# Optimization experiments

Measured on AMD Instinct MI355X. Metric: run time of the kernel, lower is better.

Reference implementation:

```python
import jax, jax.numpy as jnp
import numpy as np

L, H, E, CUTOFF = 3, 128, 20, 5.0
N_NODES, N_EDGES = 10000, 160000
NUM_EMBED = 119


def _linear(key, fin, fout):
    kw, kb = jax.random.split(key)
    s = 1.0 / np.sqrt(fin)
    W = jax.random.uniform(kw, (fin, fout), minval=-s, maxval=s, dtype=jnp.float32)
    b = jax.random.uniform(kb, (fout,), minval=-s, maxval=s, dtype=jnp.float32)
    return W, b


def _stack(key, fin, fout):
    Ws, bs = zip(*[_linear(k, fin, fout) for k in jax.random.split(key, L)])
    return jnp.stack(Ws), jnp.stack(bs)


def setup_inputs() -> dict:
    key = jax.random.key(0)
    ks = jax.random.split(key, 14)
    z = jax.random.randint(ks[0], (N_NODES,), 0, NUM_EMBED)
    edge = jax.random.randint(ks[1], (N_EDGES, 2), 0, N_NODES)
    edge_diff = jax.random.normal(ks[2], (N_EDGES, 3), dtype=jnp.float32) * 1.5
    edge_dist = jnp.linalg.norm(edge_diff, axis=-1) + 1e-2  # consistent unit vectors, strictly > 0
    embed = jax.random.normal(ks[3], (NUM_EMBED, H), dtype=jnp.float32)
    msg_filter_w, msg_filter_b = _stack(ks[4], E, 3 * H)
    msg_w1, msg_b1 = _stack(ks[5], H, H)
    msg_w2, msg_b2 = _stack(ks[6], H, 3 * H)
    upd_U_w, upd_U_b = _stack(ks[7], H, H)
    upd_V_w, upd_V_b = _stack(ks[8], H, H)
    upd_w1, upd_b1 = _stack(ks[9], 2 * H, H)
    upd_w2, upd_b2 = _stack(ks[10], H, 3 * H)
    ro_w1, ro_b1 = _linear(ks[11], H, H)
    ro_w2, ro_b2 = _linear(ks[12], H, H)
    return dict(z=z, edge=edge, edge_diff=edge_diff, edge_dist=edge_dist, embed=embed,
                msg_filter_w=msg_filter_w, msg_filter_b=msg_filter_b,
                msg_w1=msg_w1, msg_b1=msg_b1, msg_w2=msg_w2, msg_b2=msg_b2,
                upd_U_w=upd_U_w, upd_U_b=upd_U_b, upd_V_w=upd_V_w, upd_V_b=upd_V_b,
                upd_w1=upd_w1, upd_b1=upd_b1, upd_w2=upd_w2, upd_b2=upd_b2,
                ro_w1=ro_w1, ro_b1=ro_b1, ro_w2=ro_w2, ro_b2=ro_b2)


def _silu(x):
    return x * jax.nn.sigmoid(x)


def reference(z, edge, edge_diff, edge_dist, embed,
              msg_filter_w, msg_filter_b, msg_w1, msg_b1, msg_w2, msg_b2,
              upd_U_w, upd_U_b, upd_V_w, upd_V_b, upd_w1, upd_b1, upd_w2, upd_b2,
              ro_w1, ro_b1, ro_w2, ro_b2):
    N = z.shape[0]
    pi = jnp.asarray(np.pi, dtype=edge_dist.dtype)
    # sinc radial basis: sin(n*pi*d/cutoff)/d, n=1..E  -> [E_edges, E]
    n = jnp.arange(1, E + 1, dtype=edge_dist.dtype)
    rbf = jnp.sin(edge_dist[:, None] * n * pi / CUTOFF) / edge_dist[:, None]
    # cosine cutoff [E_edges]
    fcut = jnp.where(edge_dist < CUTOFF, 0.5 * (jnp.cos(pi * edge_dist / CUTOFF) + 1.0), 0.0)
    unit = edge_diff / edge_dist[:, None]  # [E_edges, 3]
    src = edge[:, 1]
    dst = edge[:, 0]

    node_scalar = embed[z]                                       # [N, H]
    node_vector = jnp.zeros((N, 3, H), dtype=edge_diff.dtype)    # [N, 3, H]

    for l in range(L):
        # --- message ---
        filter_w = (rbf @ msg_filter_w[l] + msg_filter_b[l]) * fcut[:, None]   # [E_edges, 3H]
        scalar_out = _silu(node_scalar @ msg_w1[l] + msg_b1[l]) @ msg_w2[l] + msg_b2[l]  # [N, 3H]
        filter_out = filter_w * scalar_out[src]                                 # gather + mul
        gate_sv, gate_ev, msg_s = jnp.split(filter_out, 3, axis=1)
        msg_v = node_vector[src] * gate_sv[:, None, :] + gate_ev[:, None, :] * unit[:, :, None]
        node_scalar = node_scalar + jax.ops.segment_sum(msg_s, dst, num_segments=N)
        node_vector = node_vector + jax.ops.segment_sum(msg_v, dst, num_segments=N)
        # --- update ---
        Uv = node_vector @ upd_U_w[l] + upd_U_b[l]   # [N, 3, H]
        Vv = node_vector @ upd_V_w[l] + upd_V_b[l]
        Vv_norm = jnp.linalg.norm(Vv, axis=1)        # [N, H]
        mlp_in = jnp.concatenate((Vv_norm, node_scalar), axis=1)
        mlp_out = _silu(mlp_in @ upd_w1[l] + upd_b1[l]) @ upd_w2[l] + upd_b2[l]
        a_vv, a_sv, a_ss = jnp.split(mlp_out, 3, axis=1)
        node_vector = node_vector + a_vv[:, None, :] * Uv
        node_scalar = node_scalar + a_sv * jnp.sum(Uv * Vv, axis=1) + a_ss

    # readout MLP
    return _silu(node_scalar @ ro_w1 + ro_b1) @ ro_w2 + ro_b2
```

## Files before the change

### kernel.cpp

```cpp
#include <hip/hip_runtime.h>
#include <hip/hip_bf16.h>

typedef __hip_bfloat16 bf16;
typedef __attribute__((ext_vector_type(8))) short bf16x8;
typedef __attribute__((ext_vector_type(4))) float f32x4;

#define H 128
#define F3H 384
#define E_RBF 20
#define NLAYER 3

__device__ __forceinline__ float silu_f(float x) { return x / (1.0f + __expf(-x)); }
__device__ __forceinline__ float b2f(bf16 x) { return __bfloat162float(x); }

constexpr float PI_F = 3.14159265358979323846f;
constexpr float CUT = 5.0f;

__global__ __launch_bounds__(256) void csr_hist(
    const int* __restrict__ edge, int* __restrict__ cnt, int nE) {
  int e = blockIdx.x * blockDim.x + threadIdx.x;
  if (e < nE) atomicAdd(&cnt[edge[2 * e]], 1);
}

__global__ __launch_bounds__(256) void csr_scan(
    const int* __restrict__ cnt, int* __restrict__ rowstart, int* __restrict__ cur, int N) {
  __shared__ int part[256];
  int t = threadIdx.x;
  int chunk = (N + 255) / 256;
  int lo = t * chunk; if (lo > N) lo = N;
  int hi = lo + chunk; if (hi > N) hi = N;
  int s = 0;
  for (int i = lo; i < hi; i++) s += cnt[i];
  part[t] = s;
  __syncthreads();
  if (t == 0) {
    int r = 0;
    for (int i = 0; i < 256; i++) { int v = part[i]; part[i] = r; r += v; }
  }
  __syncthreads();
  int r = part[t];
  for (int i = lo; i < hi; i++) { rowstart[i] = r; cur[i] = r; r += cnt[i]; }
}

__global__ __launch_bounds__(256) void csr_fill(
    const int* __restrict__ edge, int* __restrict__ cur, int* __restrict__ elist, int nE) {
  int e = blockIdx.x * blockDim.x + threadIdx.x;
  if (e < nE) {
    int d = edge[2 * e];
    int p = atomicAdd(&cur[d], 1);
    elist[p] = e;
  }
}

__global__ __launch_bounds__(256) void edge_pack(
    const int* __restrict__ elist, const int* __restrict__ edge,
    const float* __restrict__ edist, const float* __restrict__ ediff,
    int* __restrict__ srcs, float* __restrict__ geo, int nE) {
  int j = blockIdx.x * blockDim.x + threadIdx.x;
  if (j >= nE) return;
  int e = elist[j];
  srcs[j] = edge[2 * e + 1];
  float d = edist[e];
  float inv = 1.0f / d;
  float th = d * (PI_F / CUT);
  float s1 = sinf(th), c1 = cosf(th);
  float fc = (d < CUT) ? 0.5f * (c1 + 1.0f) : 0.0f;
  float* g = geo + (size_t)j * 24;
  float twoc = 2.0f * c1;
  float skp = 0.0f, sk = s1;
  #pragma unroll
  for (int k = 0; k < E_RBF; k++) {
    g[k] = sk * inv * fc;
    float nx = twoc * sk - skp;
    skp = sk; sk = nx;
  }
  g[20] = ediff[3 * (size_t)e] * inv;
  g[21] = ediff[3 * (size_t)e + 1] * inv;
  g[22] = ediff[3 * (size_t)e + 2] * inv;
  g[23] = fc;
}

__global__ __launch_bounds__(H) void node_init(
    const int* __restrict__ z, const float* __restrict__ embed,
    float* __restrict__ ns, bf16* __restrict__ ns16, int N) {
  int i = blockIdx.x;
  int h = threadIdx.x;
  float v = embed[(size_t)z[i] * H + h];
  ns[(size_t)i * H + h] = v;
  ns16[(size_t)i * H + h] = __float2bfloat16(v);
}

__global__ __launch_bounds__(256) void pack_w(
    const float* __restrict__ Wu, const float* __restrict__ Wv,
    bf16* __restrict__ wp) {
  int t = blockIdx.x * blockDim.x + threadIdx.x;
  if (t >= 3 * 2 * 4 * 8 * 64) return;
  int lane = t & 63;
  int c    = (t >> 6) & 7;
  int kb   = (t >> 9) & 3;
  int mat  = (t >> 11) & 1;
  int l    = t >> 12;
  const float* src = (mat ? Wv : Wu) + (size_t)l * H * H;
  bf16* dst = wp + ((size_t)(l * 2 + mat) * 16384) + (((kb * 8 + c) * 64 + lane) * 8);
  int quad = lane >> 4;
  int n = c * 16 + (lane & 15);
  #pragma unroll
  for (int j = 0; j < 8; j++) {
    int k = kb * 32 + quad * 8 + j;
    dst[j] = __float2bfloat16(src[(size_t)k * H + n]);
  }
}

__global__ __launch_bounds__(256) void pack_b(
    const float* __restrict__ src, bf16* __restrict__ dst,
    int K, int ncols, int L) {
  int kblocks = K >> 5, ncols16 = ncols >> 4;
  int total = L * kblocks * ncols16 * 64;
  int t = blockIdx.x * blockDim.x + threadIdx.x;
  if (t >= total) return;
  int lane = t & 63;
  int idx = t >> 6;
  int c = idx % ncols16; idx /= ncols16;
  int kb = idx % kblocks; idx /= kblocks;
  int l = idx;
  const float* s = src + (size_t)l * K * ncols;
  bf16* d = dst + (size_t)l * K * ncols + (((kb * ncols16 + c) * 64 + lane) * 8);
  int quad = lane >> 4;
  int n = c * 16 + (lane & 15);
  #pragma unroll
  for (int j = 0; j < 8; j++) {
    int k = kb * 32 + quad * 8 + j;
    d[j] = __float2bfloat16(s[(size_t)k * ncols + n]);
  }
}

__global__ __launch_bounds__(256) void mlp_msg(
    const bf16* __restrict__ A, const bf16* __restrict__ Wp1,
    const float* __restrict__ b1, const bf16* __restrict__ Wp2,
    const float* __restrict__ b2, bf16* __restrict__ so, int M) {
  __shared__ bf16 m1l[32][136];
  int wave = threadIdx.x >> 6, lane = threadIdx.x & 63;
  int rowg = wave >> 1, ch = wave & 1;
  int r0 = blockIdx.x * 32 + rowg * 16;
  int quad = lane >> 4, nn = lane & 15;
  int arow = r0 + nn; if (arow >= M) arow = M - 1;
  f32x4 acc[4] = {};
  for (int kb = 0; kb < 4; kb++) {
    bf16x8 af = *(const bf16x8*)&A[(size_t)arow * H + kb * 32 + quad * 8];
    #pragma unroll
    for (int c = 0; c < 4; c++) {
      int cg = ch * 4 + c;
      bf16x8 bw = *(const bf16x8*)&Wp1[(((kb * 8 + cg) * 64) + lane) * 8];
      acc[c] = __builtin_amdgcn_mfma_f32_16x16x32_bf16(af, bw, acc[c], 0, 0, 0);
    }
  }
  #pragma unroll
  for (int c = 0; c < 4; c++) {
    int n = (ch * 4 + c) * 16 + nn;
    float bb = b1[n];
    #pragma unroll
    for (int r = 0; r < 4; r++) {
      int lr = rowg * 16 + quad * 4 + r;
      m1l[lr][n] = __float2bfloat16(silu_f(acc[c][r] + bb));
    }
  }
  __syncthreads();
  f32x4 a0[4] = {}, a1[4] = {}, a2[4] = {};
  for (int kb = 0; kb < 4; kb++) {
    bf16x8 af = *(const bf16x8*)&m1l[rowg * 16 + nn][kb * 32 + quad * 8];
    #pragma unroll
    for (int c = 0; c < 4; c++) {
      int cg = ch * 4 + c;
      bf16x8 b0 = *(const bf16x8*)&Wp2[(((kb * 24 + cg) * 64) + lane) * 8];
      bf16x8 b1v = *(const bf16x8*)&Wp2[(((kb * 24 + cg + 8) * 64) + lane) * 8];
      bf16x8 b2v = *(const bf16x8*)&Wp2[(((kb * 24 + cg + 16) * 64) + lane) * 8];
      a0[c] = __builtin_amdgcn_mfma_f32_16x16x32_bf16(af, b0, a0[c], 0, 0, 0);
      a1[c] = __builtin_amdgcn_mfma_f32_16x16x32_bf16(af, b1v, a1[c], 0, 0, 0);
      a2[c] = __builtin_amdgcn_mfma_f32_16x16x32_bf16(af, b2v, a2[c], 0, 0, 0);
    }
  }
  #pragma unroll
  for (int c = 0; c < 4; c++) {
    int n = (ch * 4 + c) * 16 + nn;
    float bb0 = b2[n], bb1 = b2[H + n], bb2 = b2[2 * H + n];
    #pragma unroll
    for (int r = 0; r < 4; r++) {
      int row = r0 + quad * 4 + r;
      if (row < M) {
        so[(size_t)row * F3H + n]           = __float2bfloat16(a0[c][r] + bb0);
        so[(size_t)row * F3H + H + n]       = __float2bfloat16(a1[c][r] + bb1);
        so[(size_t)row * F3H + 2 * H + n]   = __float2bfloat16(a2[c][r] + bb2);
      }
    }
  }
}

__global__ __launch_bounds__(384) void uv_upd(
    const bf16* __restrict__ A, const bf16* __restrict__ Wpuv,
    const float* __restrict__ bu, const float* __restrict__ bv,
    const bf16* __restrict__ nsmsg,
    const bf16* __restrict__ Wp1, const float* __restrict__ b1,
    const bf16* __restrict__ Wp2, const float* __restrict__ b2,
    float* __restrict__ ns, bf16* __restrict__ ns16,
    float* __restrict__ nv, bf16* __restrict__ nvb16, int N) {
  __shared__ float Uv_l[96][132];
  __shared__ float Vv_l[96][132];
  __shared__ bf16 vn_l[32][136];
  __shared__ bf16 m1l[32][136];
  int wave = threadIdx.x >> 6;
  int lane = threadIdx.x & 63;
  int quad = lane >> 4, nn = lane & 15;
  int M3 = 3 * N;

  {
    int r0 = blockIdx.x * 96 + wave * 16;
    int arow = r0 + nn; if (arow >= M3) arow = M3 - 1;
    f32x4 accu[8] = {};
    f32x4 accv[8] = {};
    for (int kb = 0; kb < 4; kb++) {
      bf16x8 af = *(const bf16x8*)&A[(size_t)arow * H + kb * 32 + quad * 8];
      #pragma unroll
      for (int c = 0; c < 8; c++) {
        bf16x8 bfu = *(const bf16x8*)&Wpuv[(((kb * 8 + c) * 64) + lane) * 8];
        bf16x8 bfv = *(const bf16x8*)&Wpuv[16384 + (((kb * 8 + c) * 64) + lane) * 8];
        accu[c] = __builtin_amdgcn_mfma_f32_16x16x32_bf16(af, bfu, accu[c], 0, 0, 0);
        accv[c] = __builtin_amdgcn_mfma_f32_16x16x32_bf16(af, bfv, accv[c], 0, 0, 0);
      }
    }
    #pragma unroll
    for (int c = 0; c < 8; c++) {
      int n = c * 16 + nn;
      float bub = bu[n], bvb = bv[n];
      #pragma unroll
      for (int r = 0; r < 4; r++) {
        int lr = wave * 16 + quad * 4 + r;
        Uv_l[lr][n] = accu[c][r] + bub;
        Vv_l[lr][n] = accv[c][r] + bvb;
      }
    }
  }
  __syncthreads();

  for (int t = threadIdx.x; t < 32 * H; t += 384) {
    int node = t >> 7, hh = t & 127;
    float v0 = Vv_l[node * 3][hh];
    float v1 = Vv_l[node * 3 + 1][hh];
    float v2 = Vv_l[node * 3 + 2][hh];
    vn_l[node][hh] = __float2bfloat16(sqrtf(v0 * v0 + v1 * v1 + v2 * v2));
  }
  __syncthreads();

  int rowg = wave >> 1, ch = wave & 1;
  int r0n = blockIdx.x * 32 + rowg * 16;
  int arown = r0n + nn; if (arown >= N) arown = N - 1;
  if (wave < 4) {
    f32x4 acc[4] = {};
    for (int kb = 0; kb < 8; kb++) {
      bf16x8 af;
      if (kb < 4) af = *(const bf16x8*)&vn_l[rowg * 16 + nn][kb * 32 + quad * 8];
      else        af = *(const bf16x8*)&nsmsg[(size_t)arown * H + (kb - 4) * 32 + quad * 8];
      #pragma unroll
      for (int c = 0; c < 4; c++) {
        int cg = ch * 4 + c;
        bf16x8 bw = *(const bf16x8*)&Wp1[(((kb * 8 + cg) * 64) + lane) * 8];
        acc[c] = __builtin_amdgcn_mfma_f32_16x16x32_bf16(af, bw, acc[c], 0, 0, 0);
      }
    }
    #pragma unroll
    for (int c = 0; c < 4; c++) {
      int n = (ch * 4 + c) * 16 + nn;
      float bb = b1[n];
      #pragma unroll
      for (int r = 0; r < 4; r++) {
        int lr = rowg * 16 + quad * 4 + r;
        m1l[lr][n] = __float2bfloat16(silu_f(acc[c][r] + bb));
      }
    }
  }
  __syncthreads();

  if (wave < 4) {
    f32x4 aav[4] = {}, aas[4] = {}, asz[4] = {};
    for (int kb = 0; kb < 4; kb++) {
      bf16x8 af = *(const bf16x8*)&m1l[rowg * 16 + nn][kb * 32 + quad * 8];
      #pragma unroll
      for (int c = 0; c < 4; c++) {
        int cg = ch * 4 + c;
        bf16x8 b0 = *(const bf16x8*)&Wp2[(((kb * 24 + cg) * 64) + lane) * 8];
        bf16x8 b1v = *(const bf16x8*)&Wp2[(((kb * 24 + cg + 8) * 64) + lane) * 8];
        bf16x8 b2v = *(const bf16x8*)&Wp2[(((kb * 24 + cg + 16) * 64) + lane) * 8];
        aav[c] = __builtin_amdgcn_mfma_f32_16x16x32_bf16(af, b0, aav[c], 0, 0, 0);
        aas[c] = __builtin_amdgcn_mfma_f32_16x16x32_bf16(af, b1v, aas[c], 0, 0, 0);
        asz[c] = __builtin_amdgcn_mfma_f32_16x16x32_bf16(af, b2v, asz[c], 0, 0, 0);
      }
    }
    #pragma unroll
    for (int c = 0; c < 4; c++) {
      int n = (ch * 4 + c) * 16 + nn;
      float bav = b2[n], bas = b2[H + n], bss = b2[2 * H + n];
      #pragma unroll
      for (int r = 0; r < 4; r++) {
        int row = r0n + quad * 4 + r;
        if (row < N) {
          int lrn = rowg * 16 + quad * 4 + r;
          float avv = aav[c][r] + bav;
          float asv = aas[c][r] + bas;
          float ass = asz[c][r] + bss;
          float u0 = Uv_l[lrn * 3 + 0][n];
          float u1 = Uv_l[lrn * 3 + 1][n];
          float u2 = Uv_l[lrn * 3 + 2][n];
          float v0 = Vv_l[lrn * 3 + 0][n];
          float v1 = Vv_l[lrn * 3 + 1][n];
          float v2 = Vv_l[lrn * 3 + 2][n];
          float dot = u0 * v0 + u1 * v1 + u2 * v2;
          float ns_new = ns[(size_t)row * H + n] + asv * dot + ass;
          ns[(size_t)row * H + n] = ns_new;
          ns16[(size_t)row * H + n] = __float2bfloat16(ns_new);
          float n0 = nv[(size_t)(3 * row + 0) * H + n] + avv * u0;
          float n1 = nv[(size_t)(3 * row + 1) * H + n] + avv * u1;
          float n2 = nv[(size_t)(3 * row + 2) * H + n] + avv * u2;
          nv[(size_t)(3 * row + 0) * H + n] = n0;
          nv[(size_t)(3 * row + 1) * H + n] = n1;
          nv[(size_t)(3 * row + 2) * H + n] = n2;
          nvb16[(size_t)(3 * row + 0) * H + n] = __float2bfloat16(n0);
          nvb16[(size_t)(3 * row + 1) * H + n] = __float2bfloat16(n1);
          nvb16[(size_t)(3 * row + 2) * H + n] = __float2bfloat16(n2);
        }
      }
    }
  }
}

__global__ __launch_bounds__(256) void mlp_ro(
    const bf16* __restrict__ A, const bf16* __restrict__ Wp1,
    const float* __restrict__ b1, const bf16* __restrict__ Wp2,
    const float* __restrict__ b2, float* __restrict__ out, int M) {
  __shared__ bf16 m1l[32][136];
  int wave = threadIdx.x >> 6, lane = threadIdx.x & 63;
  int rowg = wave >> 1, ch = wave & 1;
  int r0 = blockIdx.x * 32 + rowg * 16;
  int quad = lane >> 4, nn = lane & 15;
  int arow = r0 + nn; if (arow >= M) arow = M - 1;
  f32x4 acc[4] = {};
  for (int kb = 0; kb < 4; kb++) {
    bf16x8 af = *(const bf16x8*)&A[(size_t)arow * H + kb * 32 + quad * 8];
    #pragma unroll
    for (int c = 0; c < 4; c++) {
      int cg = ch * 4 + c;
      bf16x8 bw = *(const bf16x8*)&Wp1[(((kb * 8 + cg) * 64) + lane) * 8];
      acc[c] = __builtin_amdgcn_mfma_f32_16x16x32_bf16(af, bw, acc[c], 0, 0, 0);
    }
  }
  #pragma unroll
  for (int c = 0; c < 4; c++) {
    int n = (ch * 4 + c) * 16 + nn;
    float bb = b1[n];
    #pragma unroll
    for (int r = 0; r < 4; r++) {
      int lr = rowg * 16 + quad * 4 + r;
      m1l[lr][n] = __float2bfloat16(silu_f(acc[c][r] + bb));
    }
  }
  __syncthreads();
  f32x4 a2[4] = {};
  for (int kb = 0; kb < 4; kb++) {
    bf16x8 af = *(const bf16x8*)&m1l[rowg * 16 + nn][kb * 32 + quad * 8];
    #pragma unroll
    for (int c = 0; c < 4; c++) {
      int cg = ch * 4 + c;
      bf16x8 bw = *(const bf16x8*)&Wp2[(((kb * 8 + cg) * 64) + lane) * 8];
      a2[c] = __builtin_amdgcn_mfma_f32_16x16x32_bf16(af, bw, a2[c], 0, 0, 0);
    }
  }
  #pragma unroll
  for (int c = 0; c < 4; c++) {
    int n = (ch * 4 + c) * 16 + nn;
    float bb = b2[n];
    #pragma unroll
    for (int r = 0; r < 4; r++) {
      int row = r0 + quad * 4 + r;
      if (row < M) out[(size_t)row * H + n] = a2[c][r] + bb;
    }
  }
}

template<bool HASNV>
__global__ __launch_bounds__(128, 4) void message3(
    const int* __restrict__ srcs, const int* __restrict__ rowstart,
    const int* __restrict__ cnt, const float* __restrict__ geo,
    const float* __restrict__ Wf, const float* __restrict__ bfb,
    const bf16* __restrict__ so, const bf16* __restrict__ nvb16,
    const float* __restrict__ nvA,
    float* __restrict__ ns, float* __restrict__ nvB,
    bf16* __restrict__ nvmsg16, bf16* __restrict__ nsmsg, int N) {
  int i = blockIdx.x;
  int h = threadIdx.x;

  float wf0[E_RBF], wf1[E_RBF], wf2[E_RBF];
  #pragma unroll
  for (int k = 0; k < E_RBF; k++) {
    wf0[k] = Wf[k * F3H + h];
    wf1[k] = Wf[k * F3H + H + h];
    wf2[k] = Wf[k * F3H + 2 * H + h];
  }
  float bb0 = bfb[h], bb1 = bfb[H + h], bb2 = bfb[2 * H + h];

  float accs = 0.0f, a0 = 0.0f, a1 = 0.0f, a2 = 0.0f;
  int jlo = rowstart[i], jhi = jlo + cnt[i];
  int j = jlo;
  for (; j + 1 < jhi; j += 2) {
    int s0 = srcs[j];
    int s1 = srcs[j + 1];
    const bf16* sop0 = so + (size_t)s0 * F3H;
    const bf16* sop1 = so + (size_t)s1 * F3H;
    float sA0 = b2f(sop0[h]), sB0 = b2f(sop0[H + h]), sC0 = b2f(sop0[2 * H + h]);
    float sA1 = b2f(sop1[h]), sB1 = b2f(sop1[H + h]), sC1 = b2f(sop1[2 * H + h]);
    float nA0, nB0, nC0, nA1, nB1, nC1;
    if (HASNV) {
      const bf16* nvp0 = nvb16 + (size_t)s0 * F3H;
      const bf16* nvp1 = nvb16 + (size_t)s1 * F3H;
      nA0 = b2f(nvp0[h]); nB0 = b2f(nvp0[H + h]); nC0 = b2f(nvp0[2 * H + h]);
      nA1 = b2f(nvp1[h]); nB1 = b2f(nvp1[H + h]); nC1 = b2f(nvp1[2 * H + h]);
    }

    {
      const float* g = geo + (size_t)j * 24;
      float gg[24];
      #pragma unroll
      for (int q = 0; q < 6; q++) *(float4*)&gg[4 * q] = *(const float4*)&g[4 * q];
      float fc = gg[23];
      float f0 = bb0 * fc, f1 = bb1 * fc, f2 = bb2 * fc;
      #pragma unroll
      for (int k = 0; k < E_RBF; k++) {
        float rk = gg[k];
        f0 += rk * wf0[k];
        f1 += rk * wf1[k];
        f2 += rk * wf2[k];
      }
      float u0 = gg[20], u1 = gg[21], u2 = gg[22];
      float gsv = f0 * sA0;
      float gev = f1 * sB0;
      accs += f2 * sC0;
      if (HASNV) {
        a0 += nA0 * gsv + gev * u0;
        a1 += nB0 * gsv + gev * u1;
        a2 += nC0 * gsv + gev * u2;
      } else {
        a0 += gev * u0;
        a1 += gev * u1;
        a2 += gev * u2;
      }
    }
    {
      const float* g = geo + (size_t)(j + 1) * 24;
      float gg[24];
      #pragma unroll
      for (int q = 0; q < 6; q++) *(float4*)&gg[4 * q] = *(const float4*)&g[4 * q];
      float fc = gg[23];
      float f0 = bb0 * fc, f1 = bb1 * fc, f2 = bb2 * fc;
      #pragma unroll
      for (int k = 0; k < E_RBF; k++) {
        float rk = gg[k];
        f0 += rk * wf0[k];
        f1 += rk * wf1[k];
        f2 += rk * wf2[k];
      }
      float u0 = gg[20], u1 = gg[21], u2 = gg[22];
      float gsv = f0 * sA1;
      float gev = f1 * sB1;
      accs += f2 * sC1;
      if (HASNV) {
        a0 += nA1 * gsv + gev * u0;
        a1 += nB1 * gsv + gev * u1;
        a2 += nC1 * gsv + gev * u2;
      } else {
        a0 += gev * u0;
        a1 += gev * u1;
        a2 += gev * u2;
      }
    }
  }
  if (j < jhi) {
    int src = srcs[j];
    const float* g = geo + (size_t)j * 24;
    float gg[24];
    #pragma unroll
    for (int q = 0; q < 6; q++) *(float4*)&gg[4 * q] = *(const float4*)&g[4 * q];
    float fc = gg[23];
    float f0 = bb0 * fc, f1 = bb1 * fc, f2 = bb2 * fc;
    #pragma unroll
    for (int k = 0; k < E_RBF; k++) {
      float rk = gg[k];
      f0 += rk * wf0[k];
      f1 += rk * wf1[k];
      f2 += rk * wf2[k];
    }
    float u0 = gg[20], u1 = gg[21], u2 = gg[22];
    const bf16* sop = so + (size_t)src * F3H;
    float gsv = f0 * b2f(sop[h]);
    float gev = f1 * b2f(sop[H + h]);
    accs += f2 * b2f(sop[2 * H + h]);
    if (HASNV) {
      const bf16* nvp = nvb16 + (size_t)src * F3H;
      a0 += b2f(nvp[h])         * gsv + gev * u0;
      a1 += b2f(nvp[H + h])     * gsv + gev * u1;
      a2 += b2f(nvp[2 * H + h]) * gsv + gev * u2;
    } else {
      a0 += gev * u0;
      a1 += gev * u1;
      a2 += gev * u2;
    }
  }

  float ns_new = ns[(size_t)i * H + h] + accs;
  ns[(size_t)i * H + h] = ns_new;
  nsmsg[(size_t)i * H + h] = __float2bfloat16(ns_new);
  float o0, o1, o2;
  if (HASNV) {
    const float* nvi = nvA + (size_t)i * F3H;
    o0 = nvi[h] + a0;
    o1 = nvi[H + h] + a1;
    o2 = nvi[2 * H + h] + a2;
  } else {
    o0 = a0; o1 = a1; o2 = a2;
  }
  nvB[(size_t)i * F3H + h]         = o0;
  nvB[(size_t)i * F3H + H + h]     = o1;
  nvB[(size_t)i * F3H + 2 * H + h] = o2;
  nvmsg16[(size_t)i * F3H + h]         = __float2bfloat16(o0);
  nvmsg16[(size_t)i * F3H + H + h]     = __float2bfloat16(o1);
  nvmsg16[(size_t)i * F3H + 2 * H + h] = __float2bfloat16(o2);
}

extern "C" void kernel_launch(void* const* d_in, const int* in_sizes, int n_in,
                              void* d_out, int out_size, void* d_ws, size_t ws_size,
                              hipStream_t stream) {
  const int*   z     = (const int*)d_in[0];
  const int*   edge  = (const int*)d_in[1];
  const float* ediff = (const float*)d_in[2];
  const float* edist = (const float*)d_in[3];
  const float* embed = (const float*)d_in[4];
  const float* mfw   = (const float*)d_in[5];
  const float* mfb   = (const float*)d_in[6];
  const float* mw1   = (const float*)d_in[7];
  const float* mb1   = (const float*)d_in[8];
  const float* mw2   = (const float*)d_in[9];
  const float* mb2   = (const float*)d_in[10];
  const float* uUw   = (const float*)d_in[11];
  const float* uUb   = (const float*)d_in[12];
  const float* uVw   = (const float*)d_in[13];
  const float* uVb   = (const float*)d_in[14];
  const float* uw1   = (const float*)d_in[15];
  const float* ub1   = (const float*)d_in[16];
  const float* uw2   = (const float*)d_in[17];
  const float* ub2   = (const float*)d_in[18];
  const float* rw1   = (const float*)d_in[19];
  const float* rb1   = (const float*)d_in[20];
  const float* rw2   = (const float*)d_in[21];
  const float* rb2   = (const float*)d_in[22];

  const int N  = in_sizes[0];
  const int nE = in_sizes[3];

  float* ws = (float*)d_ws;
  size_t off = 0;
  float* ns      = ws + off; off += (size_t)N * H;
  float* nvA     = ws + off; off += (size_t)N * F3H;
  float* nvB     = ws + off; off += (size_t)N * F3H;
  float* geo     = ws + off; off += (size_t)nE * 24;
  bf16* so       = (bf16*)(ws + off); off += (size_t)N * F3H / 2;
  bf16* nvb16    = (bf16*)(ws + off); off += (size_t)N * F3H / 2;
  bf16* nvmsg16  = (bf16*)(ws + off); off += (size_t)N * F3H / 2;
  bf16* nsmsg    = (bf16*)(ws + off); off += (size_t)N * 64;
  bf16* ns16     = (bf16*)(ws + off); off += (size_t)N * 64;
  bf16* wpack    = (bf16*)(ws + off); off += 3 * 2 * 16384 / 2;
  bf16* wp_m1    = (bf16*)(ws + off); off += 3 * 256 * 128 / 2;
  bf16* wp_m2    = (bf16*)(ws + off); off += 3 * 128 * 384 / 2;
  bf16* wp_sm1   = (bf16*)(ws + off); off += 3 * 128 * 128 / 2;
  bf16* wp_sm2   = (bf16*)(ws + off); off += 3 * 128 * 384 / 2;
  bf16* wp_ro1   = (bf16*)(ws + off); off += 128 * 128 / 2;
  bf16* wp_ro2   = (bf16*)(ws + off); off += 128 * 128 / 2;
  int* srcs     = (int*)(ws + off); off += nE;
  int* cnt      = (int*)(ws + off); off += N;
  int* rowstart = (int*)(ws + off); off += N;
  int* cur      = (int*)(ws + off); off += N;
  int* elist    = (int*)(ws + off); off += nE;

  const int tilesN = (N + 31) / 32;

  (void)hipMemsetAsync(cnt, 0, (size_t)N * sizeof(int), stream);
  csr_hist<<<(nE + 255) / 256, 256, 0, stream>>>(edge, cnt, nE);
  csr_scan<<<1, 256, 0, stream>>>(cnt, rowstart, cur, N);
  csr_fill<<<(nE + 255) / 256, 256, 0, stream>>>(edge, cur, elist, nE);
  edge_pack<<<(nE + 255) / 256, 256, 0, stream>>>(elist, edge, edist, ediff, srcs, geo, nE);
  pack_w<<<48, 256, 0, stream>>>(uUw, uVw, wpack);
  pack_b<<<48, 256, 0, stream>>>(uw1, wp_m1, 256, 128, 3);
  pack_b<<<72, 256, 0, stream>>>(uw2, wp_m2, 128, 384, 3);
  pack_b<<<24, 256, 0, stream>>>(mw1, wp_sm1, 128, 128, 3);
  pack_b<<<72, 256, 0, stream>>>(mw2, wp_sm2, 128, 384, 3);
  pack_b<<<8, 256, 0, stream>>>(rw1, wp_ro1, 128, 128, 1);
  pack_b<<<8, 256, 0, stream>>>(rw2, wp_ro2, 128, 128, 1);

  node_init<<<N, H, 0, stream>>>(z, embed, ns, ns16, N);

  float* nv_cur = nvA;
  float* nv_nxt = nvB;
  for (int l = 0; l < NLAYER; l++) {
    mlp_msg<<<tilesN, 256, 0, stream>>>(
        ns16, wp_sm1 + (size_t)l * 128 * 128, mb1 + (size_t)l * H,
        wp_sm2 + (size_t)l * 128 * 384, mb2 + (size_t)l * F3H, so, N);

    if (l == 0)
      message3<false><<<N, H, 0, stream>>>(srcs, rowstart, cnt, geo,
                                           mfw + (size_t)l * E_RBF * F3H, mfb + (size_t)l * F3H,
                                           so, nvb16, nv_cur, ns, nv_nxt, nvmsg16, nsmsg, N);
    else
      message3<true><<<N, H, 0, stream>>>(srcs, rowstart, cnt, geo,
                                          mfw + (size_t)l * E_RBF * F3H, mfb + (size_t)l * F3H,
                                          so, nvb16, nv_cur, ns, nv_nxt, nvmsg16, nsmsg, N);

    uv_upd<<<tilesN, 384, 0, stream>>>(
        nvmsg16, wpack + (size_t)l * 2 * 16384,
        uUb + (size_t)l * H, uVb + (size_t)l * H,
        nsmsg,
        wp_m1 + (size_t)l * 256 * 128, ub1 + (size_t)l * H,
        wp_m2 + (size_t)l * 128 * 384, ub2 + (size_t)l * F3H,
        ns, ns16, nv_nxt, nvb16, N);

    float* t = nv_cur; nv_cur = nv_nxt; nv_nxt = t;
  }

  mlp_ro<<<tilesN, 256, 0, stream>>>(
      ns16, wp_ro1, rb1, wp_ro2, rb2, (float*)d_out, N);
}
```

Before: 516.6 us.

## Merge setup kernels, fuse CSR fill with edge packing, parallelize scan

Nine small setup launches (weight packing, node init, memset) are merged into one grid-stride pack_all kernel. The CSR fill and edge geometry packing become one kernel that writes directly to the atomically claimed slot, which removes the elist indirection. The single-block scan now uses 1024 threads and a parallel Hillis-Steele prefix sum in place of a serial loop on thread 0. The aim is to cut launch overhead and serial setup time, at the cost of geometry writes being scattered by atomic slot position.

```diff
diff --git a/kernel.cpp b/kernel.cpp
--- a/kernel.cpp
+++ b/kernel.cpp
@@ -22,50 +22,42 @@
   if (e < nE) atomicAdd(&cnt[edge[2 * e]], 1);
 }
 
-__global__ __launch_bounds__(256) void csr_scan(
+__global__ __launch_bounds__(1024) void csr_scan(
     const int* __restrict__ cnt, int* __restrict__ rowstart, int* __restrict__ cur, int N) {
-  __shared__ int part[256];
+  __shared__ int part[1024];
   int t = threadIdx.x;
-  int chunk = (N + 255) / 256;
+  int chunk = (N + 1023) / 1024;
   int lo = t * chunk; if (lo > N) lo = N;
   int hi = lo + chunk; if (hi > N) hi = N;
   int s = 0;
   for (int i = lo; i < hi; i++) s += cnt[i];
   part[t] = s;
   __syncthreads();
-  if (t == 0) {
-    int r = 0;
-    for (int i = 0; i < 256; i++) { int v = part[i]; part[i] = r; r += v; }
-  }
-  __syncthreads();
-  int r = part[t];
+  for (int off = 1; off < 1024; off <<= 1) {
+    int v = (t >= off) ? part[t - off] : 0;
+    __syncthreads();
+    part[t] += v;
+    __syncthreads();
+  }
+  int r = (t == 0) ? 0 : part[t - 1];
   for (int i = lo; i < hi; i++) { rowstart[i] = r; cur[i] = r; r += cnt[i]; }
 }
 
-__global__ __launch_bounds__(256) void csr_fill(
-    const int* __restrict__ edge, int* __restrict__ cur, int* __restrict__ elist, int nE) {
-  int e = blockIdx.x * blockDim.x + threadIdx.x;
-  if (e < nE) {
-    int d = edge[2 * e];
-    int p = atomicAdd(&cur[d], 1);
-    elist[p] = e;
-  }
-}
-
-__global__ __launch_bounds__(256) void edge_pack(
-    const int* __restrict__ elist, const int* __restrict__ edge,
+__global__ __launch_bounds__(256) void csr_fill_pack(
+    const int* __restrict__ edge, int* __restrict__ cur,
     const float* __restrict__ edist, const float* __restrict__ ediff,
     int* __restrict__ srcs, float* __restrict__ geo, int nE) {
-  int j = blockIdx.x * blockDim.x + threadIdx.x;
-  if (j >= nE) return;
-  int e = elist[j];
-  srcs[j] = edge[2 * e + 1];
-  float d = edist[e];
-  float inv = 1.0f / d;
-  float th = d * (PI_F / CUT);
+  int e = blockIdx.x * blockDim.x + threadIdx.x;
+  if (e >= nE) return;
+  int d = edge[2 * e];
+  int p = atomicAdd(&cur[d], 1);
+  srcs[p] = edge[2 * e + 1];
+  float dd = edist[e];
+  float inv = 1.0f / dd;
+  float th = dd * (PI_F / CUT);
   float s1 = sinf(th), c1 = cosf(th);
-  float fc = (d < CUT) ? 0.5f * (c1 + 1.0f) : 0.0f;
-  float* g = geo + (size_t)j * 24;
+  float fc = (dd < CUT) ? 0.5f * (c1 + 1.0f) : 0.0f;
+  float* g = geo + (size_t)p * 24;
   float twoc = 2.0f * c1;
   float skp = 0.0f, sk = s1;
   #pragma unroll
@@ -80,21 +72,9 @@
   g[23] = fc;
 }
 
-__global__ __launch_bounds__(H) void node_init(
-    const int* __restrict__ z, const float* __restrict__ embed,
-    float* __restrict__ ns, bf16* __restrict__ ns16, int N) {
-  int i = blockIdx.x;
-  int h = threadIdx.x;
-  float v = embed[(size_t)z[i] * H + h];
-  ns[(size_t)i * H + h] = v;
-  ns16[(size_t)i * H + h] = __float2bfloat16(v);
-}
-
-__global__ __launch_bounds__(256) void pack_w(
+__device__ __forceinline__ void pack_w_item(
     const float* __restrict__ Wu, const float* __restrict__ Wv,
-    bf16* __restrict__ wp) {
-  int t = blockIdx.x * blockDim.x + threadIdx.x;
-  if (t >= 3 * 2 * 4 * 8 * 64) return;
+    bf16* __restrict__ wp, int t) {
   int lane = t & 63;
   int c    = (t >> 6) & 7;
   int kb   = (t >> 9) & 3;
@@ -111,13 +91,10 @@
   }
 }
 
-__global__ __launch_bounds__(256) void pack_b(
+__device__ __forceinline__ void pack_b_item(
     const float* __restrict__ src, bf16* __restrict__ dst,
-    int K, int ncols, int L) {
+    int K, int ncols, int t) {
   int kblocks = K >> 5, ncols16 = ncols >> 4;
-  int total = L * kblocks * ncols16 * 64;
-  int t = blockIdx.x * blockDim.x + threadIdx.x;
-  if (t >= total) return;
   int lane = t & 63;
   int idx = t >> 6;
   int c = idx % ncols16; idx /= ncols16;
@@ -131,6 +108,46 @@
   for (int j = 0; j < 8; j++) {
     int k = kb * 32 + quad * 8 + j;
     d[j] = __float2bfloat16(s[(size_t)k * ncols + n]);
+  }
+}
+
+__global__ __launch_bounds__(256) void pack_all(
+    const float* __restrict__ Wu, const float* __restrict__ Wv, bf16* __restrict__ wpack,
+    const float* __restrict__ uw1, bf16* __restrict__ wp_m1,
+    const float* __restrict__ uw2, bf16* __restrict__ wp_m2,
+    const float* __restrict__ mw1, bf16* __restrict__ wp_sm1,
+    const float* __restrict__ mw2, bf16* __restrict__ wp_sm2,
+    const float* __restrict__ rw1, bf16* __restrict__ wp_ro1,
+    const float* __restrict__ rw2, bf16* __restrict__ wp_ro2,
+    const int* __restrict__ z, const float* __restrict__ embed,
+    float* __restrict__ ns, bf16* __restrict__ ns16,
+    int* __restrict__ cnt, int N) {
+  const int T0 = 12288;
+  const int T1 = T0 + 12288;
+  const int T2 = T1 + 18432;
+  const int T3 = T2 + 6144;
+  const int T4 = T3 + 18432;
+  const int T5 = T4 + 2048;
+  const int T6 = T5 + 2048;
+  const int TN = T6 + N * H;
+  const int TT = TN + N;
+  for (int t = blockIdx.x * blockDim.x + threadIdx.x; t < TT; t += gridDim.x * blockDim.x) {
+    if (t < T0)      pack_w_item(Wu, Wv, wpack, t);
+    else if (t < T1) pack_b_item(uw1, wp_m1, 256, 128, t - T0);
+    else if (t < T2) pack_b_item(uw2, wp_m2, 128, 384, t - T1);
+    else if (t < T3) pack_b_item(mw1, wp_sm1, 128, 128, t - T2);
+    else if (t < T4) pack_b_item(mw2, wp_sm2, 128, 384, t - T3);
+    else if (t < T5) pack_b_item(rw1, wp_ro1, 128, 128, t - T4);
+    else if (t < T6) pack_b_item(rw2, wp_ro2, 128, 128, t - T5);
+    else if (t < TN) {
+      int u = t - T6;
+      int i = u >> 7, h = u & 127;
+      float v = embed[(size_t)z[i] * H + h];
+      ns[(size_t)i * H + h] = v;
+      ns16[(size_t)i * H + h] = __float2bfloat16(v);
+    } else {
+      cnt[t - TN] = 0;
+    }
   }
 }
 
@@ -584,24 +601,15 @@
   int* cnt      = (int*)(ws + off); off += N;
   int* rowstart = (int*)(ws + off); off += N;
   int* cur      = (int*)(ws + off); off += N;
-  int* elist    = (int*)(ws + off); off += nE;
 
   const int tilesN = (N + 31) / 32;
 
-  (void)hipMemsetAsync(cnt, 0, (size_t)N * sizeof(int), stream);
+  pack_all<<<1024, 256, 0, stream>>>(
+      uUw, uVw, wpack, uw1, wp_m1, uw2, wp_m2, mw1, wp_sm1, mw2, wp_sm2,
+      rw1, wp_ro1, rw2, wp_ro2, z, embed, ns, ns16, cnt, N);
   csr_hist<<<(nE + 255) / 256, 256, 0, stream>>>(edge, cnt, nE);
-  csr_scan<<<1, 256, 0, stream>>>(cnt, rowstart, cur, N);
-  csr_fill<<<(nE + 255) / 256, 256, 0, stream>>>(edge, cur, elist, nE);
-  edge_pack<<<(nE + 255) / 256, 256, 0, stream>>>(elist, edge, edist, ediff, srcs, geo, nE);
-  pack_w<<<48, 256, 0, stream>>>(uUw, uVw, wpack);
-  pack_b<<<48, 256, 0, stream>>>(uw1, wp_m1, 256, 128, 3);
-  pack_b<<<72, 256, 0, stream>>>(uw2, wp_m2, 128, 384, 3);
-  pack_b<<<24, 256, 0, stream>>>(mw1, wp_sm1, 128, 128, 3);
-  pack_b<<<72, 256, 0, stream>>>(mw2, wp_sm2, 128, 384, 3);
-  pack_b<<<8, 256, 0, stream>>>(rw1, wp_ro1, 128, 128, 1);
-  pack_b<<<8, 256, 0, stream>>>(rw2, wp_ro2, 128, 128, 1);
-
-  node_init<<<N, H, 0, stream>>>(z, embed, ns, ns16, N);
+  csr_scan<<<1, 1024, 0, stream>>>(cnt, rowstart, cur, N);
+  csr_fill_pack<<<(nE + 255) / 256, 256, 0, stream>>>(edge, cur, edist, ediff, srcs, geo, nE);
 
   float* nv_cur = nvA;
   float* nv_nxt = nvB;
```

Result: faster. 483.2 us (-6.5%).
